# Performance work log

Measured on AMD Instinct MI355X. Metric: run time of the kernel, lower is better.

## Reference

```python
import jax, jax.numpy as jnp
from jax import lax
import numpy as np

CHANNELS = 16
THRESH = 0.1
UPDATE_RATE = 0.25


def _sobel_kernel():
    ident = np.array([[0., 0., 0.], [0., 1., 0.], [0., 0., 0.]], np.float32)
    sx = np.array([[-1., 0., 1.], [-2., 0., 2.], [-1., 0., 1.]], np.float32)
    sy = sx.T
    k = np.stack([ident, sx, sy])[:, None, :, :]          # [3,1,3,3]
    k = np.tile(k, (CHANNELS, 1, 1, 1))                   # [48,1,3,3] (torch repeat order)
    return jnp.asarray(k)


def _perceive(x, w_sobel):
    # circular pad then depthwise grouped conv (groups=CHANNELS, 3 filters per group)
    xp = jnp.pad(x, ((0, 0), (0, 0), (1, 1), (1, 1)), mode='wrap')
    return lax.conv_general_dilated(
        xp, w_sobel, window_strides=(1, 1), padding='VALID',
        dimension_numbers=('NCHW', 'OIHW', 'NCHW'),
        feature_group_count=CHANNELS)                     # [B,48,H,W]


def _alive_mask(x):
    alpha = x[:, 3:4]                                     # [B,1,H,W]
    p = jnp.pad(alpha, ((0, 0), (0, 0), (1, 1), (1, 1)), mode='wrap')
    m = lax.reduce_window(p, -jnp.inf, lax.max, (1, 1, 3, 3), (1, 1, 1, 1), 'VALID')
    return (m > THRESH).astype(x.dtype)


def _mlp(y, w1, b1, w2, b2, w3):
    h = jax.nn.relu(jnp.einsum('bchw,oc->bohw', y, w1) + b1[None, :, None, None])
    h = jax.nn.relu(jnp.einsum('bchw,oc->bohw', h, w2) + b2[None, :, None, None])
    return jnp.einsum('bchw,oc->bohw', h, w3)             # [B,16,H,W], no bias


def setup_inputs() -> dict:
    key = jax.random.key(0)
    ks = jax.random.split(key, 7)
    B, H, W, steps = 8, 256, 256, 2
    s = 0.1
    return {
        'x': jax.random.uniform(ks[0], (B, CHANNELS, H, W), jnp.float32),
        'w1': jax.random.normal(ks[1], (64, 48), jnp.float32) * s,
        'b1': jax.random.normal(ks[2], (64,), jnp.float32) * s,
        'w2': jax.random.normal(ks[3], (64, 64), jnp.float32) * s,
        'b2': jax.random.normal(ks[4], (64,), jnp.float32) * s,
        'w3': jax.random.normal(ks[5], (CHANNELS, 64), jnp.float32) * s,
        'update_masks': jax.random.uniform(ks[6], (steps, B, 1, H, W), jnp.float32),
        'steps': steps,
    }


def reference(x, w1, b1, w2, b2, w3, update_masks, steps):
    w_sobel = _sobel_kernel()
    for i in range(steps):
        pre = _alive_mask(x)
        y = _mlp(_perceive(x, w_sobel), w1, b1, w2, b2, w3)
        um = (update_masks[i] < UPDATE_RATE).astype(x.dtype)
        x = x + y * um
        post = _alive_mask(x)
        x = x * (pre * post)
    return x
```

## Files before the change

kernel.cpp:

```cpp
#include <hip/hip_runtime.h>
#include <hip/hip_bf16.h>

#define NB 8
#define NC 16
#define NH 256
#define NW 256
#define ALIVE_THRESH 0.1f
#define UPDATE_RATE 0.25f

typedef __attribute__((ext_vector_type(8))) short bf16x8;
typedef __attribute__((ext_vector_type(4))) float f32x4;
typedef unsigned short ushort_t;

#define MFMA16(a, b, c) __builtin_amdgcn_mfma_f32_16x16x32_bf16((a), (b), (c), 0, 0, 0)

static __device__ __forceinline__ unsigned short f2bf(float f) {
    __hip_bfloat16 h = __float2bfloat16(f);
    return __builtin_bit_cast(unsigned short, h);
}
static __device__ __forceinline__ float bf2f(unsigned short b) {
    union { unsigned u; float f; } x; x.u = ((unsigned)b) << 16; return x.f;
}
static __device__ __forceinline__ unsigned pack2(float lo, float hi) {
    return (unsigned)f2bf(lo) | ((unsigned)f2bf(hi) << 16);
}
static __device__ __forceinline__ float bfbits(unsigned w, int hi) {
    return bf2f((unsigned short)(hi ? (w >> 16) : (w & 0xffffu)));
}

static __device__ __forceinline__ int ybyte(int px, int g) {
    return px * 128 + ((g ^ (px & 7)) << 4);
}

__global__ void prep_weights(const float* __restrict__ w1, const float* __restrict__ b1,
                             const float* __restrict__ w2, const float* __restrict__ w3,
                             int4* __restrict__ wf)
{
    const int f = blockIdx.x, l = threadIdx.x;
    const int lq = l >> 4, ln = l & 15;
    union { unsigned short us[8]; int4 v; } u;
    if (f < 8) {
        const int mt = f >> 1, ks = f & 1, m = mt * 16 + ln;
        #pragma unroll
        for (int j = 0; j < 8; ++j) {
            const int k = ks * 32 + lq * 8 + j;
            float v = (k < 48) ? w1[m * 48 + k] : ((k == 48) ? b1[m] : 0.0f);
            u.us[j] = f2bf(v);
        }
    } else if (f < 16) {
        const int ff = f - 8, mt = ff >> 1, ks = ff & 1, m = mt * 16 + ln;
        #pragma unroll
        for (int j = 0; j < 8; ++j)
            u.us[j] = f2bf(w2[m * 64 + (ks * 32 + lq * 8 + j)]);
    } else {
        const int ks = f - 16, m = ln;
        #pragma unroll
        for (int j = 0; j < 8; ++j)
            u.us[j] = f2bf(w3[m * 64 + (ks * 32 + lq * 8 + j)]);
    }
    wf[f * 64 + l] = u.v;
}

template<typename ResF, typename OutF>
static __device__ __forceinline__ void mlp_gemm(
    char* yb, int lane, int px0,
    const int4* __restrict__ wf, const float* __restrict__ b2,
    const float* __restrict__ umr, ResF getres, OutF putout)
{
    const int lq = lane >> 4, ln = lane & 15;

    float umv[4];
    #pragma unroll
    for (int nt = 0; nt < 4; ++nt)
        umv[nt] = (umr[px0 + nt * 16 + ln] < UPDATE_RATE) ? 1.0f : 0.0f;

    bf16x8 a1f[8];
    #pragma unroll
    for (int f = 0; f < 8; ++f)
        a1f[f] = __builtin_bit_cast(bf16x8, wf[f * 64 + lane]);

    #pragma unroll
    for (int nt = 0; nt < 4; ++nt) {
        const int px = px0 + nt * 16 + ln;
        bf16x8 bb0 = *(const bf16x8*)(yb + ybyte(px, lq));
        bf16x8 bb1 = *(const bf16x8*)(yb + ybyte(px, 4 + lq));
        #pragma unroll
        for (int mt = 0; mt < 4; ++mt) {
            f32x4 z = {0.f, 0.f, 0.f, 0.f};
            z = MFMA16(a1f[2 * mt],     bb0, z);
            z = MFMA16(a1f[2 * mt + 1], bb1, z);
            union { unsigned w[2]; uint2 v; } pk;
            pk.w[0] = pack2(fmaxf(z[0], 0.f), fmaxf(z[1], 0.f));
            pk.w[1] = pack2(fmaxf(z[2], 0.f), fmaxf(z[3], 0.f));
            *(uint2*)(yb + ybyte(px, 2 * mt + (lq >> 1)) + (lq & 1) * 8) = pk.v;
        }
    }

    bf16x8 a2f[8];
    #pragma unroll
    for (int f = 0; f < 8; ++f)
        a2f[f] = __builtin_bit_cast(bf16x8, wf[(8 + f) * 64 + lane]);
    f32x4 b2v[4];
    #pragma unroll
    for (int mt = 0; mt < 4; ++mt)
        b2v[mt] = *(const f32x4*)(b2 + mt * 16 + lq * 4);

    #pragma unroll
    for (int nt = 0; nt < 4; ++nt) {
        const int px = px0 + nt * 16 + ln;
        bf16x8 bb0 = *(const bf16x8*)(yb + ybyte(px, lq));
        bf16x8 bb1 = *(const bf16x8*)(yb + ybyte(px, 4 + lq));
        #pragma unroll
        for (int mt = 0; mt < 4; ++mt) {
            f32x4 z = {0.f, 0.f, 0.f, 0.f};
            z = MFMA16(a2f[2 * mt],     bb0, z);
            z = MFMA16(a2f[2 * mt + 1], bb1, z);
            z = z + b2v[mt];
            union { unsigned w[2]; uint2 v; } pk;
            pk.w[0] = pack2(fmaxf(z[0], 0.f), fmaxf(z[1], 0.f));
            pk.w[1] = pack2(fmaxf(z[2], 0.f), fmaxf(z[3], 0.f));
            *(uint2*)(yb + ybyte(px, 2 * mt + (lq >> 1)) + (lq & 1) * 8) = pk.v;
        }
    }

    bf16x8 a3f0 = __builtin_bit_cast(bf16x8, wf[16 * 64 + lane]);
    bf16x8 a3f1 = __builtin_bit_cast(bf16x8, wf[17 * 64 + lane]);

    #pragma unroll
    for (int nt = 0; nt < 4; ++nt) {
        const int px = px0 + nt * 16 + ln;
        bf16x8 bb0 = *(const bf16x8*)(yb + ybyte(px, lq));
        bf16x8 bb1 = *(const bf16x8*)(yb + ybyte(px, 4 + lq));
        f32x4 z = {0.f, 0.f, 0.f, 0.f};
        z = MFMA16(a3f0, bb0, z);
        z = MFMA16(a3f1, bb1, z);
        f32x4 res = getres(px, lq, nt);
        #pragma unroll
        for (int r = 0; r < 4; ++r)
            putout(px, lq, r, res[r] + z[r] * umv[nt]);
    }
}

__global__ __launch_bounds__(256) void nca_first(
    const float* __restrict__ x,
    const float* __restrict__ um,
    const int4*  __restrict__ wf,
    const float* __restrict__ b2,
    ushort_t* __restrict__ xout,
    unsigned char* __restrict__ preb_out)
{
    __shared__ char smem[256 * 128];
    char*     yb = smem;
    unsigned* sd = (unsigned*)smem;

    const int t = threadIdx.x, bx = blockIdx.x;
    const int h = ((bx & 7) << 5) | (bx >> 3);
    const int b = blockIdx.y;
    const int hm = (h - 1) & 255, hp = (h + 1) & 255;
    const size_t cs = (size_t)NH * NW;
    const size_t base = (size_t)b * NC * cs;

    {
        const float* a3p = x + base + 3 * cs;
        float mx = -1e30f;
        #pragma unroll
        for (int r = 0; r < 3; ++r) {
            const float* rp = a3p + (size_t)((h - 1 + r) & 255) * NW;
            #pragma unroll
            for (int d = 0; d < 3; ++d)
                mx = fmaxf(mx, rp[(t - 1 + d) & 255]);
        }
        preb_out[((size_t)b * NH + h) * NW + t] = (mx > ALIVE_THRESH) ? 1 : 0;
    }

    float mreg[NC], dreg[NC];
    #pragma unroll
    for (int c = 0; c < NC; ++c) {
        const float* xc = x + base + (size_t)c * cs;
        float top = xc[(size_t)hm * NW + t];
        float mid = xc[(size_t)h  * NW + t];
        float bot = xc[(size_t)hp * NW + t];
        sd[c * NW + t] = pack2(top + 2.0f * mid + bot, bot - top);
        mreg[c] = mid; dreg[c] = bot - top;
    }
    __syncthreads();

    const int tm = (t - 1) & 255, tp = (t + 1) & 255;
    unsigned yp[24];
    {
        unsigned short ys[48];
        #pragma unroll
        for (int c = 0; c < NC; ++c) {
            unsigned L = sd[c * NW + tm], R = sd[c * NW + tp];
            float sl = bfbits(L, 0), dl = bfbits(L, 1);
            float sr = bfbits(R, 0), dr = bfbits(R, 1);
            ys[3 * c + 0] = f2bf(mreg[c]);
            ys[3 * c + 1] = f2bf(sr - sl);
            ys[3 * c + 2] = f2bf(dl + 2.0f * dreg[c] + dr);
        }
        #pragma unroll
        for (int i = 0; i < 24; ++i)
            yp[i] = (unsigned)ys[2 * i] | ((unsigned)ys[2 * i + 1] << 16);
    }
    __syncthreads();

    #pragma unroll
    for (int g = 0; g < 6; ++g) {
        union { unsigned w[4]; int4 v; } pk;
        pk.w[0] = yp[4 * g]; pk.w[1] = yp[4 * g + 1];
        pk.w[2] = yp[4 * g + 2]; pk.w[3] = yp[4 * g + 3];
        *(int4*)(yb + ybyte(t, g)) = pk.v;
    }
    { int4 br; br.x = 0x3F80; br.y = 0; br.z = 0; br.w = 0;
      *(int4*)(yb + ybyte(t, 6)) = br; }
    { int4 zz; zz.x = zz.y = zz.z = zz.w = 0;
      *(int4*)(yb + ybyte(t, 7)) = zz; }

    const int lane = t & 63, wv = t >> 6;
    const float* umr = um + ((size_t)b * NH + h) * NW;

    auto getres = [&](int px, int lq, int) -> f32x4 {
        f32x4 r;
        #pragma unroll
        for (int i = 0; i < 4; ++i)
            r[i] = x[base + (size_t)(lq * 4 + i) * cs + (size_t)h * NW + px];
        return r;
    };
    auto putout = [&](int px, int lq, int r, float v) {
        xout[base + (size_t)(lq * 4 + r) * cs + (size_t)h * NW + px] = f2bf(v);
    };
    mlp_gemm(yb, lane, wv * 64, wf, b2, umr, getres, putout);
}

__global__ __launch_bounds__(256) void nca_step(
    const ushort_t* __restrict__ xin,
    const unsigned char* __restrict__ preb_in,
    const float* __restrict__ um,
    const int4*  __restrict__ wf,
    const float* __restrict__ b2,
    ushort_t* __restrict__ xout,
    unsigned char* __restrict__ preb_out)
{
    __shared__ char smem[256 * 128];
    char*     yb = smem;
    unsigned* sd = (unsigned*)smem;

    const int t = threadIdx.x, bx = blockIdx.x;
    const int h = ((bx & 7) << 5) | (bx >> 3);
    const int b = blockIdx.y;
    const int hm = (h - 1) & 255, hp = (h + 1) & 255;
    const size_t cs = (size_t)NH * NW;
    const size_t base = (size_t)b * NC * cs;
    const size_t prow = (size_t)b * NH;

    float a[5][5];
    {
        const ushort_t* a3p = xin + base + 3 * cs;
        #pragma unroll
        for (int j = 0; j < 5; ++j) {
            const ushort_t* rp = a3p + (size_t)((h - 2 + j) & 255) * NW;
            #pragma unroll
            for (int d = 0; d < 5; ++d)
                a[j][d] = bf2f(rp[(t - 2 + d) & 255]);
        }
    }

    float m3x3[3][3];
    #pragma unroll
    for (int r = 0; r < 3; ++r) {
        float cm[5];
        #pragma unroll
        for (int d = 0; d < 5; ++d)
            cm[d] = fmaxf(fmaxf(a[r][d], a[r + 1][d]), a[r + 2][d]);
        #pragma unroll
        for (int dd = 0; dd < 3; ++dd) {
            float post = fmaxf(fmaxf(cm[dd], cm[dd + 1]), cm[dd + 2]);
            const int hh = (h - 1 + r) & 255, uu = (t - 1 + dd) & 255;
            unsigned char p = preb_in[(prow + hh) * NW + uu];
            m3x3[r][dd] = (post > ALIVE_THRESH && p) ? 1.0f : 0.0f;
        }
    }

    {
        float pm = 0.0f;
        #pragma unroll
        for (int r = 0; r < 3; ++r)
            #pragma unroll
            for (int dd = 0; dd < 3; ++dd)
                pm = fmaxf(pm, a[1 + r][1 + dd] * m3x3[r][dd]);
        preb_out[(prow + h) * NW + t] = (pm > ALIVE_THRESH) ? 1 : 0;
    }

    const float m0 = m3x3[0][1], m1 = m3x3[1][1], m2 = m3x3[2][1];

    float mreg[NC], dreg[NC];
    #pragma unroll
    for (int c = 0; c < NC; ++c) {
        float top, mid, bot;
        if (c == 3) { top = a[1][2] * m0; mid = a[2][2] * m1; bot = a[3][2] * m2; }
        else {
            const ushort_t* xc = xin + base + (size_t)c * cs;
            top = bf2f(xc[(size_t)hm * NW + t]) * m0;
            mid = bf2f(xc[(size_t)h  * NW + t]) * m1;
            bot = bf2f(xc[(size_t)hp * NW + t]) * m2;
        }
        sd[c * NW + t] = pack2(top + 2.0f * mid + bot, bot - top);
        mreg[c] = mid; dreg[c] = bot - top;
    }
    __syncthreads();

    const int tm = (t - 1) & 255, tp = (t + 1) & 255;
    unsigned yp[24];
    {
        unsigned short ys[48];
        #pragma unroll
        for (int c = 0; c < NC; ++c) {
            unsigned L = sd[c * NW + tm], R = sd[c * NW + tp];
            float sl = bfbits(L, 0), dl = bfbits(L, 1);
            float sr = bfbits(R, 0), dr = bfbits(R, 1);
            ys[3 * c + 0] = f2bf(mreg[c]);
            ys[3 * c + 1] = f2bf(sr - sl);
            ys[3 * c + 2] = f2bf(dl + 2.0f * dreg[c] + dr);
        }
        #pragma unroll
        for (int i = 0; i < 24; ++i)
            yp[i] = (unsigned)ys[2 * i] | ((unsigned)ys[2 * i + 1] << 16);
    }
    __syncthreads();

    #pragma unroll
    for (int g = 0; g < 6; ++g) {
        union { unsigned w[4]; int4 v; } pk;
        pk.w[0] = yp[4 * g]; pk.w[1] = yp[4 * g + 1];
        pk.w[2] = yp[4 * g + 2]; pk.w[3] = yp[4 * g + 3];
        *(int4*)(yb + ybyte(t, g)) = pk.v;
    }
    { int4 br; br.x = 0x3F80; br.y = 0; br.z = 0; br.w = 0;
      *(int4*)(yb + ybyte(t, 6)) = br; }
    { int4 zz; zz.x = zz.y = zz.z = zz.w = 0;
      *(int4*)(yb + ybyte(t, 7)) = zz; }

    const int lane = t & 63, wv = t >> 6;
    const float* umr = um + (prow + h) * NW;

    auto getres = [&](int px, int lq, int) -> f32x4 {
        const float mm = __shfl(m1, px & 63);
        f32x4 r;
        #pragma unroll
        for (int i = 0; i < 4; ++i)
            r[i] = bf2f(xin[base + (size_t)(lq * 4 + i) * cs + (size_t)h * NW + px]) * mm;
        return r;
    };
    auto putout = [&](int px, int lq, int r, float v) {
        xout[base + (size_t)(lq * 4 + r) * cs + (size_t)h * NW + px] = f2bf(v);
    };
    mlp_gemm(yb, lane, wv * 64, wf, b2, umr, getres, putout);
}

__global__ __launch_bounds__(256) void nca_final(
    const ushort_t* __restrict__ xin,
    const unsigned char* __restrict__ preb,
    float* __restrict__ xout)
{
    const int t = threadIdx.x, bx = blockIdx.x;
    const int h = ((bx & 7) << 5) | (bx >> 3);
    const int b = blockIdx.y;
    const size_t cs = (size_t)NH * NW;
    const size_t base = (size_t)b * NC * cs;

    const ushort_t* a3p = xin + base + 3 * cs;
    float mx = -1e30f;
    #pragma unroll
    for (int r = 0; r < 3; ++r) {
        const ushort_t* rp = a3p + (size_t)((h - 1 + r) & 255) * NW;
        #pragma unroll
        for (int d = 0; d < 3; ++d)
            mx = fmaxf(mx, bf2f(rp[(t - 1 + d) & 255]));
    }
    const float m = (mx > ALIVE_THRESH && preb[((size_t)b * NH + h) * NW + t])
                        ? 1.0f : 0.0f;

    const size_t off = (size_t)h * NW + t;
    #pragma unroll
    for (int c = 0; c < NC; ++c)
        xout[base + (size_t)c * cs + off] = bf2f(xin[base + (size_t)c * cs + off]) * m;
}

extern "C" void kernel_launch(void* const* d_in, const int* in_sizes, int n_in,
                              void* d_out, int out_size, void* d_ws, size_t ws_size,
                              hipStream_t stream) {
    const float* x  = (const float*)d_in[0];
    const float* w1 = (const float*)d_in[1];
    const float* b1 = (const float*)d_in[2];
    const float* w2 = (const float*)d_in[3];
    const float* b2 = (const float*)d_in[4];
    const float* w3 = (const float*)d_in[5];
    const float* um = (const float*)d_in[6];
    const int steps = in_sizes[6] / (NB * NH * NW);

    const size_t npix  = (size_t)NB * NH * NW;
    const size_t nelem = (size_t)NB * NC * NH * NW;

    ushort_t* bfA        = (ushort_t*)d_ws;
    ushort_t* bfB        = bfA + nelem;
    unsigned char* prebA = (unsigned char*)(bfB + nelem);
    unsigned char* prebB = prebA + npix;
    int4* wf             = (int4*)(prebB + npix);
    float* xout          = (float*)d_out;

    prep_weights<<<18, 64, 0, stream>>>(w1, b1, w2, w3, wf);

    dim3 grd(NH, NB);

    const ushort_t* cur = bfA;
    unsigned char* preb_last = prebA;

    for (int i = 0; i < steps; ++i) {
        const float* um_i = um + (size_t)i * npix;
        ushort_t* bfo      = (i % 2 == 0) ? bfA : bfB;
        unsigned char* po  = (i % 2 == 0) ? prebA : prebB;
        unsigned char* pin = (i % 2 == 0) ? prebB : prebA;

        if (i == 0)
            nca_first<<<grd, 256, 0, stream>>>(x, um_i, wf, b2, bfo, po);
        else
            nca_step<<<grd, 256, 0, stream>>>(cur, pin, um_i, wf, b2, bfo, po);
        cur = bfo;
        preb_last = po;
    }

    nca_final<<<grd, 256, 0, stream>>>(cur, preb_last, xout);
}
```

Measured before the change: 64.49 us.

## Store intermediate NCA state pixel-interleaved with separate alpha plane

```diff
diff --git a/kernel.cpp b/kernel.cpp
--- a/kernel.cpp
+++ b/kernel.cpp
@@ -28,6 +28,10 @@
     return bf2f((unsigned short)(hi ? (w >> 16) : (w & 0xffffu)));
 }
 
+#define W16(q0, q1, i) ((i) == 0 ? (q0).x : (i) == 1 ? (q0).y : (i) == 2 ? (q0).z : \
+                        (i) == 3 ? (q0).w : (i) == 4 ? (q1).x : (i) == 5 ? (q1).y : \
+                        (i) == 6 ? (q1).z : (q1).w)
+
 static __device__ __forceinline__ int ybyte(int px, int g) {
     return px * 128 + ((g ^ (px & 7)) << 4);
 }
@@ -59,6 +63,42 @@
             u.us[j] = f2bf(w3[m * 64 + (ks * 32 + lq * 8 + j)]);
     }
     wf[f * 64 + l] = u.v;
+}
+
+static __device__ __forceinline__ void combine_store(
+    char* yb, unsigned* sd, int t, const float* mreg, const float* dreg)
+{
+    __syncthreads();
+    const int tm = (t - 1) & 255, tp = (t + 1) & 255;
+    unsigned yp[24];
+    {
+        unsigned short ys[48];
+        #pragma unroll
+        for (int c = 0; c < NC; ++c) {
+            unsigned L = sd[c * NW + tm], R = sd[c * NW + tp];
+            float sl = bfbits(L, 0), dl = bfbits(L, 1);
+            float sr = bfbits(R, 0), dr = bfbits(R, 1);
+            ys[3 * c + 0] = f2bf(mreg[c]);
+            ys[3 * c + 1] = f2bf(sr - sl);
+            ys[3 * c + 2] = f2bf(dl + 2.0f * dreg[c] + dr);
+        }
+        #pragma unroll
+        for (int i = 0; i < 24; ++i)
+            yp[i] = (unsigned)ys[2 * i] | ((unsigned)ys[2 * i + 1] << 16);
+    }
+    __syncthreads();
+
+    #pragma unroll
+    for (int g = 0; g < 6; ++g) {
+        union { unsigned w[4]; int4 v; } pk;
+        pk.w[0] = yp[4 * g]; pk.w[1] = yp[4 * g + 1];
+        pk.w[2] = yp[4 * g + 2]; pk.w[3] = yp[4 * g + 3];
+        *(int4*)(yb + ybyte(t, g)) = pk.v;
+    }
+    { int4 br; br.x = 0x3F80; br.y = 0; br.z = 0; br.w = 0;
+      *(int4*)(yb + ybyte(t, 6)) = br; }
+    { int4 zz; zz.x = zz.y = zz.z = zz.w = 0;
+      *(int4*)(yb + ybyte(t, 7)) = zz; }
 }
 
 template<typename ResF, typename OutF>
@@ -135,18 +175,21 @@
         z = MFMA16(a3f0, bb0, z);
         z = MFMA16(a3f1, bb1, z);
         f32x4 res = getres(px, lq, nt);
+        f32x4 out;
         #pragma unroll
         for (int r = 0; r < 4; ++r)
-            putout(px, lq, r, res[r] + z[r] * umv[nt]);
-    }
-}
-
-__global__ __launch_bounds__(256) void nca_first(
+            out[r] = res[r] + z[r] * umv[nt];
+        putout(px, lq, out);
+    }
+}
+
+__global__ __launch_bounds__(256, 4) void nca_first(
     const float* __restrict__ x,
     const float* __restrict__ um,
     const int4*  __restrict__ wf,
     const float* __restrict__ b2,
-    ushort_t* __restrict__ xout,
+    ushort_t* __restrict__ ps_out,
+    ushort_t* __restrict__ sc_out,
     unsigned char* __restrict__ preb_out)
 {
     __shared__ char smem[256 * 128];
@@ -159,6 +202,7 @@
     const int hm = (h - 1) & 255, hp = (h + 1) & 255;
     const size_t cs = (size_t)NH * NW;
     const size_t base = (size_t)b * NC * cs;
+    const size_t prow = (size_t)b * NH;
 
     {
         const float* a3p = x + base + 3 * cs;
@@ -170,7 +214,7 @@
             for (int d = 0; d < 3; ++d)
                 mx = fmaxf(mx, rp[(t - 1 + d) & 255]);
         }
-        preb_out[((size_t)b * NH + h) * NW + t] = (mx > ALIVE_THRESH) ? 1 : 0;
+        preb_out[(prow + h) * NW + t] = (mx > ALIVE_THRESH) ? 1 : 0;
     }
 
     float mreg[NC], dreg[NC];
@@ -183,41 +227,11 @@
         sd[c * NW + t] = pack2(top + 2.0f * mid + bot, bot - top);
         mreg[c] = mid; dreg[c] = bot - top;
     }
-    __syncthreads();
-
-    const int tm = (t - 1) & 255, tp = (t + 1) & 255;
-    unsigned yp[24];
-    {
-        unsigned short ys[48];
-        #pragma unroll
-        for (int c = 0; c < NC; ++c) {
-            unsigned L = sd[c * NW + tm], R = sd[c * NW + tp];
-            float sl = bfbits(L, 0), dl = bfbits(L, 1);
-            float sr = bfbits(R, 0), dr = bfbits(R, 1);
-            ys[3 * c + 0] = f2bf(mreg[c]);
-            ys[3 * c + 1] = f2bf(sr - sl);
-            ys[3 * c + 2] = f2bf(dl + 2.0f * dreg[c] + dr);
-        }
-        #pragma unroll
-        for (int i = 0; i < 24; ++i)
-            yp[i] = (unsigned)ys[2 * i] | ((unsigned)ys[2 * i + 1] << 16);
-    }
-    __syncthreads();
-
-    #pragma unroll
-    for (int g = 0; g < 6; ++g) {
-        union { unsigned w[4]; int4 v; } pk;
-        pk.w[0] = yp[4 * g]; pk.w[1] = yp[4 * g + 1];
-        pk.w[2] = yp[4 * g + 2]; pk.w[3] = yp[4 * g + 3];
-        *(int4*)(yb + ybyte(t, g)) = pk.v;
-    }
-    { int4 br; br.x = 0x3F80; br.y = 0; br.z = 0; br.w = 0;
-      *(int4*)(yb + ybyte(t, 6)) = br; }
-    { int4 zz; zz.x = zz.y = zz.z = zz.w = 0;
-      *(int4*)(yb + ybyte(t, 7)) = zz; }
+
+    combine_store(yb, sd, t, mreg, dreg);
 
     const int lane = t & 63, wv = t >> 6;
-    const float* umr = um + ((size_t)b * NH + h) * NW;
+    const float* umr = um + (prow + h) * NW;
 
     auto getres = [&](int px, int lq, int) -> f32x4 {
         f32x4 r;
@@ -226,19 +240,26 @@
             r[i] = x[base + (size_t)(lq * 4 + i) * cs + (size_t)h * NW + px];
         return r;
     };
-    auto putout = [&](int px, int lq, int r, float v) {
-        xout[base + (size_t)(lq * 4 + r) * cs + (size_t)h * NW + px] = f2bf(v);
+    auto putout = [&](int px, int lq, f32x4 v) {
+        unsigned lo = pack2(v[0], v[1]);
+        unsigned hi = pack2(v[2], v[3]);
+        uint2 u; u.x = lo; u.y = hi;
+        *(uint2*)(ps_out + ((prow + h) * NW + px) * 16 + lq * 4) = u;
+        if (lq == 0)
+            sc_out[(prow + h) * NW + px] = (ushort_t)(hi >> 16);
     };
     mlp_gemm(yb, lane, wv * 64, wf, b2, umr, getres, putout);
 }
 
-__global__ __launch_bounds__(256) void nca_step(
-    const ushort_t* __restrict__ xin,
+__global__ __launch_bounds__(256, 4) void nca_step(
+    const ushort_t* __restrict__ ps_in,
+    const ushort_t* __restrict__ sc_in,
     const unsigned char* __restrict__ preb_in,
     const float* __restrict__ um,
     const int4*  __restrict__ wf,
     const float* __restrict__ b2,
-    ushort_t* __restrict__ xout,
+    ushort_t* __restrict__ ps_out,
+    ushort_t* __restrict__ sc_out,
     unsigned char* __restrict__ preb_out)
 {
     __shared__ char smem[256 * 128];
@@ -249,16 +270,13 @@
     const int h = ((bx & 7) << 5) | (bx >> 3);
     const int b = blockIdx.y;
     const int hm = (h - 1) & 255, hp = (h + 1) & 255;
-    const size_t cs = (size_t)NH * NW;
-    const size_t base = (size_t)b * NC * cs;
     const size_t prow = (size_t)b * NH;
 
     float a[5][5];
     {
-        const ushort_t* a3p = xin + base + 3 * cs;
         #pragma unroll
         for (int j = 0; j < 5; ++j) {
-            const ushort_t* rp = a3p + (size_t)((h - 2 + j) & 255) * NW;
+            const ushort_t* rp = sc_in + (prow + ((h - 2 + j) & 255)) * NW;
             #pragma unroll
             for (int d = 0; d < 5; ++d)
                 a[j][d] = bf2f(rp[(t - 2 + d) & 255]);
@@ -293,72 +311,50 @@
 
     const float m0 = m3x3[0][1], m1 = m3x3[1][1], m2 = m3x3[2][1];
 
+    const uint4* pm4 = (const uint4*)(ps_in + ((prow + hm) * NW + t) * 16);
+    const uint4* pc4 = (const uint4*)(ps_in + ((prow + h ) * NW + t) * 16);
+    const uint4* pp4 = (const uint4*)(ps_in + ((prow + hp) * NW + t) * 16);
+    uint4 qa0 = pm4[0], qa1 = pm4[1];
+    uint4 qb0 = pc4[0], qb1 = pc4[1];
+    uint4 qc0 = pp4[0], qc1 = pp4[1];
+
     float mreg[NC], dreg[NC];
     #pragma unroll
     for (int c = 0; c < NC; ++c) {
-        float top, mid, bot;
-        if (c == 3) { top = a[1][2] * m0; mid = a[2][2] * m1; bot = a[3][2] * m2; }
-        else {
-            const ushort_t* xc = xin + base + (size_t)c * cs;
-            top = bf2f(xc[(size_t)hm * NW + t]) * m0;
-            mid = bf2f(xc[(size_t)h  * NW + t]) * m1;
-            bot = bf2f(xc[(size_t)hp * NW + t]) * m2;
-        }
+        float top = bfbits(W16(qa0, qa1, c >> 1), c & 1) * m0;
+        float mid = bfbits(W16(qb0, qb1, c >> 1), c & 1) * m1;
+        float bot = bfbits(W16(qc0, qc1, c >> 1), c & 1) * m2;
         sd[c * NW + t] = pack2(top + 2.0f * mid + bot, bot - top);
         mreg[c] = mid; dreg[c] = bot - top;
     }
-    __syncthreads();
-
-    const int tm = (t - 1) & 255, tp = (t + 1) & 255;
-    unsigned yp[24];
-    {
-        unsigned short ys[48];
-        #pragma unroll
-        for (int c = 0; c < NC; ++c) {
-            unsigned L = sd[c * NW + tm], R = sd[c * NW + tp];
-            float sl = bfbits(L, 0), dl = bfbits(L, 1);
-            float sr = bfbits(R, 0), dr = bfbits(R, 1);
-            ys[3 * c + 0] = f2bf(mreg[c]);
-            ys[3 * c + 1] = f2bf(sr - sl);
-            ys[3 * c + 2] = f2bf(dl + 2.0f * dreg[c] + dr);
-        }
-        #pragma unroll
-        for (int i = 0; i < 24; ++i)
-            yp[i] = (unsigned)ys[2 * i] | ((unsigned)ys[2 * i + 1] << 16);
-    }
-    __syncthreads();
-
-    #pragma unroll
-    for (int g = 0; g < 6; ++g) {
-        union { unsigned w[4]; int4 v; } pk;
-        pk.w[0] = yp[4 * g]; pk.w[1] = yp[4 * g + 1];
-        pk.w[2] = yp[4 * g + 2]; pk.w[3] = yp[4 * g + 3];
-        *(int4*)(yb + ybyte(t, g)) = pk.v;
-    }
-    { int4 br; br.x = 0x3F80; br.y = 0; br.z = 0; br.w = 0;
-      *(int4*)(yb + ybyte(t, 6)) = br; }
-    { int4 zz; zz.x = zz.y = zz.z = zz.w = 0;
-      *(int4*)(yb + ybyte(t, 7)) = zz; }
+
+    combine_store(yb, sd, t, mreg, dreg);
 
     const int lane = t & 63, wv = t >> 6;
     const float* umr = um + (prow + h) * NW;
 
     auto getres = [&](int px, int lq, int) -> f32x4 {
         const float mm = __shfl(m1, px & 63);
+        uint2 v = *(const uint2*)(ps_in + ((prow + h) * NW + px) * 16 + lq * 4);
         f32x4 r;
-        #pragma unroll
-        for (int i = 0; i < 4; ++i)
-            r[i] = bf2f(xin[base + (size_t)(lq * 4 + i) * cs + (size_t)h * NW + px]) * mm;
+        r[0] = bfbits(v.x, 0) * mm; r[1] = bfbits(v.x, 1) * mm;
+        r[2] = bfbits(v.y, 0) * mm; r[3] = bfbits(v.y, 1) * mm;
         return r;
     };
-    auto putout = [&](int px, int lq, int r, float v) {
-        xout[base + (size_t)(lq * 4 + r) * cs + (size_t)h * NW + px] = f2bf(v);
+    auto putout = [&](int px, int lq, f32x4 v) {
+        unsigned lo = pack2(v[0], v[1]);
+        unsigned hi = pack2(v[2], v[3]);
+        uint2 u; u.x = lo; u.y = hi;
+        *(uint2*)(ps_out + ((prow + h) * NW + px) * 16 + lq * 4) = u;
+        if (lq == 0)
+            sc_out[(prow + h) * NW + px] = (ushort_t)(hi >> 16);
     };
     mlp_gemm(yb, lane, wv * 64, wf, b2, umr, getres, putout);
 }
 
 __global__ __launch_bounds__(256) void nca_final(
-    const ushort_t* __restrict__ xin,
+    const ushort_t* __restrict__ ps_in,
+    const ushort_t* __restrict__ sc_in,
     const unsigned char* __restrict__ preb,
     float* __restrict__ xout)
 {
@@ -367,23 +363,25 @@
     const int b = blockIdx.y;
     const size_t cs = (size_t)NH * NW;
     const size_t base = (size_t)b * NC * cs;
-
-    const ushort_t* a3p = xin + base + 3 * cs;
+    const size_t prow = (size_t)b * NH;
+
     float mx = -1e30f;
     #pragma unroll
     for (int r = 0; r < 3; ++r) {
-        const ushort_t* rp = a3p + (size_t)((h - 1 + r) & 255) * NW;
+        const ushort_t* rp = sc_in + (prow + ((h - 1 + r) & 255)) * NW;
         #pragma unroll
         for (int d = 0; d < 3; ++d)
             mx = fmaxf(mx, bf2f(rp[(t - 1 + d) & 255]));
     }
-    const float m = (mx > ALIVE_THRESH && preb[((size_t)b * NH + h) * NW + t])
-                        ? 1.0f : 0.0f;
+    const float m = (mx > ALIVE_THRESH && preb[(prow + h) * NW + t]) ? 1.0f : 0.0f;
+
+    const uint4* p4 = (const uint4*)(ps_in + ((prow + h) * NW + t) * 16);
+    uint4 q0 = p4[0], q1 = p4[1];
 
     const size_t off = (size_t)h * NW + t;
     #pragma unroll
     for (int c = 0; c < NC; ++c)
-        xout[base + (size_t)c * cs + off] = bf2f(xin[base + (size_t)c * cs + off]) * m;
+        xout[base + (size_t)c * cs + off] = bfbits(W16(q0, q1, c >> 1), c & 1) * m;
 }
 
 extern "C" void kernel_launch(void* const* d_in, const int* in_sizes, int n_in,
@@ -401,33 +399,43 @@
     const size_t npix  = (size_t)NB * NH * NW;
     const size_t nelem = (size_t)NB * NC * NH * NW;
 
-    ushort_t* bfA        = (ushort_t*)d_ws;
-    ushort_t* bfB        = bfA + nelem;
-    unsigned char* prebA = (unsigned char*)(bfB + nelem);
+    ushort_t* bfW        = (ushort_t*)d_ws;
+    ushort_t* scA        = bfW + nelem;
+    ushort_t* scB        = scA + npix;
+    unsigned char* prebA = (unsigned char*)(scB + npix);
     unsigned char* prebB = prebA + npix;
     int4* wf             = (int4*)(prebB + npix);
+    ushort_t* bfO        = (ushort_t*)d_out;
     float* xout          = (float*)d_out;
 
     prep_weights<<<18, 64, 0, stream>>>(w1, b1, w2, w3, wf);
 
     dim3 grd(NH, NB);
 
-    const ushort_t* cur = bfA;
+    auto stbuf = [&](int i) -> ushort_t* {
+        return (((steps - 1 - i) & 1) == 0) ? bfW : bfO;
+    };
+
+    const ushort_t* cur_ps = nullptr;
+    const ushort_t* cur_sc = nullptr;
     unsigned char* preb_last = prebA;
 
     for (int i = 0; i < steps; ++i) {
         const float* um_i = um + (size_t)i * npix;
-        ushort_t* bfo      = (i % 2 == 0) ? bfA : bfB;
+        ushort_t* pso      = stbuf(i);
+        ushort_t* sco      = (i % 2 == 0) ? scA : scB;
         unsigned char* po  = (i % 2 == 0) ? prebA : prebB;
         unsigned char* pin = (i % 2 == 0) ? prebB : prebA;
 
         if (i == 0)
-            nca_first<<<grd, 256, 0, stream>>>(x, um_i, wf, b2, bfo, po);
+            nca_first<<<grd, 256, 0, stream>>>(x, um_i, wf, b2, pso, sco, po);
         else
-            nca_step<<<grd, 256, 0, stream>>>(cur, pin, um_i, wf, b2, bfo, po);
-        cur = bfo;
+            nca_step<<<grd, 256, 0, stream>>>(cur_ps, cur_sc, pin, um_i, wf, b2,
+                                              pso, sco, po);
+        cur_ps = pso;
+        cur_sc = sco;
         preb_last = po;
     }
 
-    nca_final<<<grd, 256, 0, stream>>>(cur, preb_last, xout);
-}
+    nca_final<<<grd, 256, 0, stream>>>(cur_ps, cur_sc, preb_last, xout);
+}
```

Measured after the change: 76.75 us. 1.19x slower.

## Preload weight fragments early, shuffle update mask, vectorize final mask kernel

Applied to the files above, without the earlier changes.

```diff
diff --git a/kernel.cpp b/kernel.cpp
--- a/kernel.cpp
+++ b/kernel.cpp
@@ -32,6 +32,32 @@
     return px * 128 + ((g ^ (px & 7)) << 4);
 }
 
+struct WFrags {
+    bf16x8 a1[8];
+    bf16x8 a2[8];
+    bf16x8 a3[2];
+    f32x4  b2v[4];
+};
+
+static __device__ __forceinline__ WFrags load_wfrags(
+    const int4* __restrict__ wf, const float* __restrict__ b2, int lane)
+{
+    WFrags w;
+    #pragma unroll
+    for (int f = 0; f < 8; ++f)
+        w.a1[f] = __builtin_bit_cast(bf16x8, wf[f * 64 + lane]);
+    #pragma unroll
+    for (int f = 0; f < 8; ++f)
+        w.a2[f] = __builtin_bit_cast(bf16x8, wf[(8 + f) * 64 + lane]);
+    w.a3[0] = __builtin_bit_cast(bf16x8, wf[16 * 64 + lane]);
+    w.a3[1] = __builtin_bit_cast(bf16x8, wf[17 * 64 + lane]);
+    const int lq = lane >> 4;
+    #pragma unroll
+    for (int mt = 0; mt < 4; ++mt)
+        w.b2v[mt] = *(const f32x4*)(b2 + mt * 16 + lq * 4);
+    return w;
+}
+
 __global__ void prep_weights(const float* __restrict__ w1, const float* __restrict__ b1,
                              const float* __restrict__ w2, const float* __restrict__ w3,
                              int4* __restrict__ wf)
@@ -61,23 +87,53 @@
     wf[f * 64 + l] = u.v;
 }
 
+static __device__ __forceinline__ void combine_store(
+    char* yb, unsigned* sd, int t, const float* mreg, const float* dreg)
+{
+    __syncthreads();
+    const int tm = (t - 1) & 255, tp = (t + 1) & 255;
+    unsigned yp[24];
+    {
+        unsigned short ys[48];
+        #pragma unroll
+        for (int c = 0; c < NC; ++c) {
+            unsigned L = sd[c * NW + tm], R = sd[c * NW + tp];
+            float sl = bfbits(L, 0), dl = bfbits(L, 1);
+            float sr = bfbits(R, 0), dr = bfbits(R, 1);
+            ys[3 * c + 0] = f2bf(mreg[c]);
+            ys[3 * c + 1] = f2bf(sr - sl);
+            ys[3 * c + 2] = f2bf(dl + 2.0f * dreg[c] + dr);
+        }
+        #pragma unroll
+        for (int i = 0; i < 24; ++i)
+            yp[i] = (unsigned)ys[2 * i] | ((unsigned)ys[2 * i + 1] << 16);
+    }
+    __syncthreads();
+
+    #pragma unroll
+    for (int g = 0; g < 6; ++g) {
+        union { unsigned w[4]; int4 v; } pk;
+        pk.w[0] = yp[4 * g]; pk.w[1] = yp[4 * g + 1];
+        pk.w[2] = yp[4 * g + 2]; pk.w[3] = yp[4 * g + 3];
+        *(int4*)(yb + ybyte(t, g)) = pk.v;
+    }
+    { int4 br; br.x = 0x3F80; br.y = 0; br.z = 0; br.w = 0;
+      *(int4*)(yb + ybyte(t, 6)) = br; }
+    { int4 zz; zz.x = zz.y = zz.z = zz.w = 0;
+      *(int4*)(yb + ybyte(t, 7)) = zz; }
+}
+
 template<typename ResF, typename OutF>
 static __device__ __forceinline__ void mlp_gemm(
-    char* yb, int lane, int px0,
-    const int4* __restrict__ wf, const float* __restrict__ b2,
-    const float* __restrict__ umr, ResF getres, OutF putout)
+    char* yb, int lane, int px0, const WFrags& wfr, float um_own,
+    ResF getres, OutF putout)
 {
     const int lq = lane >> 4, ln = lane & 15;
 
     float umv[4];
     #pragma unroll
     for (int nt = 0; nt < 4; ++nt)
-        umv[nt] = (umr[px0 + nt * 16 + ln] < UPDATE_RATE) ? 1.0f : 0.0f;
-
-    bf16x8 a1f[8];
-    #pragma unroll
-    for (int f = 0; f < 8; ++f)
-        a1f[f] = __builtin_bit_cast(bf16x8, wf[f * 64 + lane]);
+        umv[nt] = (__shfl(um_own, nt * 16 + ln) < UPDATE_RATE) ? 1.0f : 0.0f;
 
     #pragma unroll
     for (int nt = 0; nt < 4; ++nt) {
@@ -87,8 +143,8 @@
         #pragma unroll
         for (int mt = 0; mt < 4; ++mt) {
             f32x4 z = {0.f, 0.f, 0.f, 0.f};
-            z = MFMA16(a1f[2 * mt],     bb0, z);
-            z = MFMA16(a1f[2 * mt + 1], bb1, z);
+            z = MFMA16(wfr.a1[2 * mt],     bb0, z);
+            z = MFMA16(wfr.a1[2 * mt + 1], bb1, z);
             union { unsigned w[2]; uint2 v; } pk;
             pk.w[0] = pack2(fmaxf(z[0], 0.f), fmaxf(z[1], 0.f));
             pk.w[1] = pack2(fmaxf(z[2], 0.f), fmaxf(z[3], 0.f));
@@ -96,15 +152,6 @@
         }
     }
 
-    bf16x8 a2f[8];
-    #pragma unroll
-    for (int f = 0; f < 8; ++f)
-        a2f[f] = __builtin_bit_cast(bf16x8, wf[(8 + f) * 64 + lane]);
-    f32x4 b2v[4];
-    #pragma unroll
-    for (int mt = 0; mt < 4; ++mt)
-        b2v[mt] = *(const f32x4*)(b2 + mt * 16 + lq * 4);
-
     #pragma unroll
     for (int nt = 0; nt < 4; ++nt) {
         const int px = px0 + nt * 16 + ln;
@@ -113,18 +160,15 @@
         #pragma unroll
         for (int mt = 0; mt < 4; ++mt) {
             f32x4 z = {0.f, 0.f, 0.f, 0.f};
-            z = MFMA16(a2f[2 * mt],     bb0, z);
-            z = MFMA16(a2f[2 * mt + 1], bb1, z);
-            z = z + b2v[mt];
+            z = MFMA16(wfr.a2[2 * mt],     bb0, z);
+            z = MFMA16(wfr.a2[2 * mt + 1], bb1, z);
+            z = z + wfr.b2v[mt];
             union { unsigned w[2]; uint2 v; } pk;
             pk.w[0] = pack2(fmaxf(z[0], 0.f), fmaxf(z[1], 0.f));
             pk.w[1] = pack2(fmaxf(z[2], 0.f), fmaxf(z[3], 0.f));
             *(uint2*)(yb + ybyte(px, 2 * mt + (lq >> 1)) + (lq & 1) * 8) = pk.v;
         }
     }
-
-    bf16x8 a3f0 = __builtin_bit_cast(bf16x8, wf[16 * 64 + lane]);
-    bf16x8 a3f1 = __builtin_bit_cast(bf16x8, wf[17 * 64 + lane]);
 
     #pragma unroll
     for (int nt = 0; nt < 4; ++nt) {
@@ -132,16 +176,16 @@
         bf16x8 bb0 = *(const bf16x8*)(yb + ybyte(px, lq));
         bf16x8 bb1 = *(const bf16x8*)(yb + ybyte(px, 4 + lq));
         f32x4 z = {0.f, 0.f, 0.f, 0.f};
-        z = MFMA16(a3f0, bb0, z);
-        z = MFMA16(a3f1, bb1, z);
-        f32x4 res = getres(px, lq, nt);
+        z = MFMA16(wfr.a3[0], bb0, z);
+        z = MFMA16(wfr.a3[1], bb1, z);
+        f32x4 res = getres(px, lq);
         #pragma unroll
         for (int r = 0; r < 4; ++r)
             putout(px, lq, r, res[r] + z[r] * umv[nt]);
     }
 }
 
-__global__ __launch_bounds__(256) void nca_first(
+__global__ __launch_bounds__(256, 3) void nca_first(
     const float* __restrict__ x,
     const float* __restrict__ um,
     const int4*  __restrict__ wf,
@@ -159,6 +203,11 @@
     const int hm = (h - 1) & 255, hp = (h + 1) & 255;
     const size_t cs = (size_t)NH * NW;
     const size_t base = (size_t)b * NC * cs;
+    const size_t prow = (size_t)b * NH;
+    const int lane = t & 63;
+
+    const WFrags wfr = load_wfrags(wf, b2, lane);
+    const float um_own = um[(prow + h) * NW + t];
 
     {
         const float* a3p = x + base + 3 * cs;
@@ -170,7 +219,7 @@
             for (int d = 0; d < 3; ++d)
                 mx = fmaxf(mx, rp[(t - 1 + d) & 255]);
         }
-        preb_out[((size_t)b * NH + h) * NW + t] = (mx > ALIVE_THRESH) ? 1 : 0;
+        preb_out[(prow + h) * NW + t] = (mx > ALIVE_THRESH) ? 1 : 0;
     }
 
     float mreg[NC], dreg[NC];
@@ -183,43 +232,12 @@
         sd[c * NW + t] = pack2(top + 2.0f * mid + bot, bot - top);
         mreg[c] = mid; dreg[c] = bot - top;
     }
-    __syncthreads();
-
-    const int tm = (t - 1) & 255, tp = (t + 1) & 255;
-    unsigned yp[24];
-    {
-        unsigned short ys[48];
-        #pragma unroll
-        for (int c = 0; c < NC; ++c) {
-            unsigned L = sd[c * NW + tm], R = sd[c * NW + tp];
-            float sl = bfbits(L, 0), dl = bfbits(L, 1);
-            float sr = bfbits(R, 0), dr = bfbits(R, 1);
-            ys[3 * c + 0] = f2bf(mreg[c]);
-            ys[3 * c + 1] = f2bf(sr - sl);
-            ys[3 * c + 2] = f2bf(dl + 2.0f * dreg[c] + dr);
-        }
-        #pragma unroll
-        for (int i = 0; i < 24; ++i)
-            yp[i] = (unsigned)ys[2 * i] | ((unsigned)ys[2 * i + 1] << 16);
-    }
-    __syncthreads();
-
-    #pragma unroll
-    for (int g = 0; g < 6; ++g) {
-        union { unsigned w[4]; int4 v; } pk;
-        pk.w[0] = yp[4 * g]; pk.w[1] = yp[4 * g + 1];
-        pk.w[2] = yp[4 * g + 2]; pk.w[3] = yp[4 * g + 3];
-        *(int4*)(yb + ybyte(t, g)) = pk.v;
-    }
-    { int4 br; br.x = 0x3F80; br.y = 0; br.z = 0; br.w = 0;
-      *(int4*)(yb + ybyte(t, 6)) = br; }
-    { int4 zz; zz.x = zz.y = zz.z = zz.w = 0;
-      *(int4*)(yb + ybyte(t, 7)) = zz; }
-
-    const int lane = t & 63, wv = t >> 6;
-    const float* umr = um + ((size_t)b * NH + h) * NW;
-
-    auto getres = [&](int px, int lq, int) -> f32x4 {
+
+    combine_store(yb, sd, t, mreg, dreg);
+
+    const int wv = t >> 6;
+
+    auto getres = [&](int px, int lq) -> f32x4 {
         f32x4 r;
         #pragma unroll
         for (int i = 0; i < 4; ++i)
@@ -229,10 +247,10 @@
     auto putout = [&](int px, int lq, int r, float v) {
         xout[base + (size_t)(lq * 4 + r) * cs + (size_t)h * NW + px] = f2bf(v);
     };
-    mlp_gemm(yb, lane, wv * 64, wf, b2, umr, getres, putout);
-}
-
-__global__ __launch_bounds__(256) void nca_step(
+    mlp_gemm(yb, lane, wv * 64, wfr, um_own, getres, putout);
+}
+
+__global__ __launch_bounds__(256, 3) void nca_step(
     const ushort_t* __restrict__ xin,
     const unsigned char* __restrict__ preb_in,
     const float* __restrict__ um,
@@ -252,6 +270,10 @@
     const size_t cs = (size_t)NH * NW;
     const size_t base = (size_t)b * NC * cs;
     const size_t prow = (size_t)b * NH;
+    const int lane = t & 63;
+
+    const WFrags wfr = load_wfrags(wf, b2, lane);
+    const float um_own = um[(prow + h) * NW + t];
 
     float a[5][5];
     {
@@ -307,43 +329,12 @@
         sd[c * NW + t] = pack2(top + 2.0f * mid + bot, bot - top);
         mreg[c] = mid; dreg[c] = bot - top;
     }
-    __syncthreads();
-
-    const int tm = (t - 1) & 255, tp = (t + 1) & 255;
-    unsigned yp[24];
-    {
-        unsigned short ys[48];
-        #pragma unroll
-        for (int c = 0; c < NC; ++c) {
-            unsigned L = sd[c * NW + tm], R = sd[c * NW + tp];
-            float sl = bfbits(L, 0), dl = bfbits(L, 1);
-            float sr = bfbits(R, 0), dr = bfbits(R, 1);
-            ys[3 * c + 0] = f2bf(mreg[c]);
-            ys[3 * c + 1] = f2bf(sr - sl);
-            ys[3 * c + 2] = f2bf(dl + 2.0f * dreg[c] + dr);
-        }
-        #pragma unroll
-        for (int i = 0; i < 24; ++i)
-            yp[i] = (unsigned)ys[2 * i] | ((unsigned)ys[2 * i + 1] << 16);
-    }
-    __syncthreads();
-
-    #pragma unroll
-    for (int g = 0; g < 6; ++g) {
-        union { unsigned w[4]; int4 v; } pk;
-        pk.w[0] = yp[4 * g]; pk.w[1] = yp[4 * g + 1];
-        pk.w[2] = yp[4 * g + 2]; pk.w[3] = yp[4 * g + 3];
-        *(int4*)(yb + ybyte(t, g)) = pk.v;
-    }
-    { int4 br; br.x = 0x3F80; br.y = 0; br.z = 0; br.w = 0;
-      *(int4*)(yb + ybyte(t, 6)) = br; }
-    { int4 zz; zz.x = zz.y = zz.z = zz.w = 0;
-      *(int4*)(yb + ybyte(t, 7)) = zz; }
-
-    const int lane = t & 63, wv = t >> 6;
-    const float* umr = um + (prow + h) * NW;
-
-    auto getres = [&](int px, int lq, int) -> f32x4 {
+
+    combine_store(yb, sd, t, mreg, dreg);
+
+    const int wv = t >> 6;
+
+    auto getres = [&](int px, int lq) -> f32x4 {
         const float mm = __shfl(m1, px & 63);
         f32x4 r;
         #pragma unroll
@@ -354,7 +345,7 @@
     auto putout = [&](int px, int lq, int r, float v) {
         xout[base + (size_t)(lq * 4 + r) * cs + (size_t)h * NW + px] = f2bf(v);
     };
-    mlp_gemm(yb, lane, wv * 64, wf, b2, umr, getres, putout);
+    mlp_gemm(yb, lane, wv * 64, wfr, um_own, getres, putout);
 }
 
 __global__ __launch_bounds__(256) void nca_final(
@@ -363,27 +354,46 @@
     float* __restrict__ xout)
 {
     const int t = threadIdx.x, bx = blockIdx.x;
-    const int h = ((bx & 7) << 5) | (bx >> 3);
     const int b = blockIdx.y;
+    const int h = (bx << 2) | (t >> 6);
+    const int px0 = (t & 63) << 2;
     const size_t cs = (size_t)NH * NW;
     const size_t base = (size_t)b * NC * cs;
+    const size_t prow = (size_t)b * NH;
 
     const ushort_t* a3p = xin + base + 3 * cs;
-    float mx = -1e30f;
+    float m0 = -1e30f, m1 = -1e30f, m2 = -1e30f, m3 = -1e30f;
     #pragma unroll
     for (int r = 0; r < 3; ++r) {
         const ushort_t* rp = a3p + (size_t)((h - 1 + r) & 255) * NW;
-        #pragma unroll
-        for (int d = 0; d < 3; ++d)
-            mx = fmaxf(mx, bf2f(rp[(t - 1 + d) & 255]));
-    }
-    const float m = (mx > ALIVE_THRESH && preb[((size_t)b * NH + h) * NW + t])
-                        ? 1.0f : 0.0f;
-
-    const size_t off = (size_t)h * NW + t;
-    #pragma unroll
-    for (int c = 0; c < NC; ++c)
-        xout[base + (size_t)c * cs + off] = bf2f(xin[base + (size_t)c * cs + off]) * m;
+        uint2 mid = *(const uint2*)(rp + px0);
+        float v0 = bfbits(mid.x, 0), v1 = bfbits(mid.x, 1);
+        float v2 = bfbits(mid.y, 0), v3 = bfbits(mid.y, 1);
+        float lm = bf2f(rp[(px0 - 1) & 255]);
+        float rm = bf2f(rp[(px0 + 4) & 255]);
+        m0 = fmaxf(m0, fmaxf(fmaxf(lm, v0), v1));
+        m1 = fmaxf(m1, fmaxf(fmaxf(v0, v1), v2));
+        m2 = fmaxf(m2, fmaxf(fmaxf(v1, v2), v3));
+        m3 = fmaxf(m3, fmaxf(fmaxf(v2, v3), rm));
+    }
+    const size_t pix = (prow + h) * NW + px0;
+    const unsigned pr4 = *(const unsigned*)(preb + pix);
+    const float f0 = (m0 > ALIVE_THRESH && (pr4 & 0x000000FFu)) ? 1.0f : 0.0f;
+    const float f1 = (m1 > ALIVE_THRESH && (pr4 & 0x0000FF00u)) ? 1.0f : 0.0f;
+    const float f2 = (m2 > ALIVE_THRESH && (pr4 & 0x00FF0000u)) ? 1.0f : 0.0f;
+    const float f3 = (m3 > ALIVE_THRESH && (pr4 & 0xFF000000u)) ? 1.0f : 0.0f;
+
+    #pragma unroll
+    for (int c = 0; c < NC; ++c) {
+        const size_t o = base + (size_t)c * cs + (size_t)h * NW + px0;
+        uint2 s = *(const uint2*)(xin + o);
+        float4 v;
+        v.x = bfbits(s.x, 0) * f0;
+        v.y = bfbits(s.x, 1) * f1;
+        v.z = bfbits(s.y, 0) * f2;
+        v.w = bfbits(s.y, 1) * f3;
+        *(float4*)(xout + o) = v;
+    }
 }
 
 extern "C" void kernel_launch(void* const* d_in, const int* in_sizes, int n_in,
@@ -411,6 +421,7 @@
     prep_weights<<<18, 64, 0, stream>>>(w1, b1, w2, w3, wf);
 
     dim3 grd(NH, NB);
+    dim3 grdF(NH / 4, NB);
 
     const ushort_t* cur = bfA;
     unsigned char* preb_last = prebA;
@@ -429,5 +440,5 @@
         preb_last = po;
     }
 
-    nca_final<<<grd, 256, 0, stream>>>(cur, preb_last, xout);
-}
+    nca_final<<<grdF, 256, 0, stream>>>(cur, preb_last, xout);
+}
```

After: 63.47 us, median of 2. About the same (-1.6%).
